# Kernel tuning notes

Hardware: AMD Instinct MI355X
Metric: run time of the kernel (lower is better)

## Reference

```python
import jax, jax.numpy as jnp
import numpy as np

RHO = 1.0
EPSILON = 0.1
N_ITERS = 5
EPS = 1e-08


def setup_inputs() -> dict:
    key = jax.random.key(0)
    k1, k2, k3 = jax.random.split(key, 3)
    B, H, M, N, D = 16, 16, 256, 576, 1024
    # student cross-attention weights: positive, rows roughly sum to 1 (post-softmax in the real model)
    sa = jax.random.uniform(k1, (B, H, M, N), dtype=jnp.float32) + 1e-3
    student_attn = sa / sa.sum(axis=-1, keepdims=True)
    visual_feats = jax.random.normal(k2, (B, N, D), dtype=jnp.float32)
    text_feats = jax.random.normal(k3, (B, M, D), dtype=jnp.float32)
    text_mask = jnp.ones((B, M), dtype=jnp.float32)
    return {"student_attn": student_attn, "visual_feats": visual_feats,
            "text_feats": text_feats, "text_mask": text_mask}


def _l2norm(x):
    return x / jnp.sqrt(jnp.sum(x * x, axis=-1, keepdims=True) + 1e-12)


def _teacher_plan(x, y, y_mask):
    # x: (B,N,D) visual, y: (B,M,D) text, y_mask: (B,M)
    B, N, D = x.shape
    M = y.shape[1]
    x_n = _l2norm(x)
    y_n = _l2norm(y)
    cost = 1.0 - jnp.einsum('bmd,bnd->bmn', y_n, x_n)          # (B,M,N)
    mu = jnp.full((B, N, 1), 1.0 / N, dtype=x.dtype)            # visual marginal (column vec)
    nu = (y_mask / (jnp.sum(y_mask, axis=1, keepdims=True) + EPS))[:, :, None]  # (B,M,1)
    K = jnp.exp(-cost / EPSILON)                                # (B,M,N)
    fi = RHO / (RHO + EPSILON)
    u = jnp.ones((B, M, 1), dtype=x.dtype)
    v = jnp.ones((B, N, 1), dtype=x.dtype)
    for _ in range(N_ITERS):
        Kv = jnp.einsum('bmn,bnk->bmk', K, v)                   # (B,M,1)
        u = (nu / (Kv + EPS)) ** fi
        Ktu = jnp.einsum('bmn,bmk->bnk', K, u)                  # (B,N,1)
        v = (mu / (Ktu + EPS)) ** fi
    P = u * K * jnp.swapaxes(v, 1, 2)                           # (B,M,N)
    return P / (jnp.sum(P, axis=-1, keepdims=True) + EPS)


def reference(student_attn, visual_feats, text_feats, text_mask):
    teacher = jax.lax.stop_gradient(_teacher_plan(visual_feats, text_feats, text_mask))
    teacher = teacher[:, None, :, :]                            # (B,1,M,N)
    loss = -jnp.sum(teacher * jnp.log(student_attn + EPS), axis=-1)  # (B,H,M)
    loss = loss * text_mask[:, None, :]
    return jnp.mean(loss)
```

## Files before the change

kernel.cpp:

```cpp
#include <hip/hip_runtime.h>
#include <math.h>

#define B_ 16
#define H_ 16
#define M_ 256
#define N_ 576
#define D_ 1024

constexpr float EPS_ = 1e-8f;
constexpr float FI_ = 0.90909090909090906f;

__device__ __forceinline__ float wave_reduce(float v) {
#pragma unroll
  for (int o = 32; o > 0; o >>= 1) v += __shfl_down(v, o, 64);
  return v;
}

__global__ __launch_bounds__(256) void rownorm_kernel(const float* __restrict__ x,
                                                      float* __restrict__ inv,
                                                      int rows) {
  int wave = (int)((blockIdx.x * blockDim.x + threadIdx.x) >> 6);
  int lane = threadIdx.x & 63;
  if (wave >= rows) return;
  const float* r = x + (size_t)wave * D_;
  float s = 0.f;
#pragma unroll
  for (int it = 0; it < 4; ++it) {
    float4 v = *(const float4*)&r[it * 256 + lane * 4];
    s += v.x * v.x + v.y * v.y + v.z * v.z + v.w * v.w;
  }
  s = wave_reduce(s);
  if (lane == 0) inv[wave] = rsqrtf(s + 1e-12f);
}

__global__ __launch_bounds__(256) void gemm_k_kernel(const float* __restrict__ vis,
                                                     const float* __restrict__ txt,
                                                     const float* __restrict__ xinv,
                                                     const float* __restrict__ yinv,
                                                     float* __restrict__ Kw) {
  __shared__ float As[16][68];
  __shared__ float Bs[16][68];
  const int b = blockIdx.z;
  const int m0 = blockIdx.y * 64;
  const int n0 = blockIdx.x * 64;
  const float* Y = txt + (size_t)b * M_ * D_;
  const float* X = vis + (size_t)b * N_ * D_;
  const int t = threadIdx.x;
  const int row = t >> 2;
  const int dl = (t & 3) << 2;
  const int tm = (t >> 4) << 2;
  const int tn = (t & 15) << 2;

  float acc[4][4] = {};
  for (int d0 = 0; d0 < D_; d0 += 16) {
    float4 ay = *(const float4*)&Y[(size_t)(m0 + row) * D_ + d0 + dl];
    float4 ax = *(const float4*)&X[(size_t)(n0 + row) * D_ + d0 + dl];
    As[dl + 0][row] = ay.x; As[dl + 1][row] = ay.y;
    As[dl + 2][row] = ay.z; As[dl + 3][row] = ay.w;
    Bs[dl + 0][row] = ax.x; Bs[dl + 1][row] = ax.y;
    Bs[dl + 2][row] = ax.z; Bs[dl + 3][row] = ax.w;
    __syncthreads();
#pragma unroll
    for (int k = 0; k < 16; ++k) {
      float4 a4 = *(const float4*)&As[k][tm];
      float4 b4 = *(const float4*)&Bs[k][tn];
      float a[4] = {a4.x, a4.y, a4.z, a4.w};
      float bb[4] = {b4.x, b4.y, b4.z, b4.w};
#pragma unroll
      for (int i = 0; i < 4; ++i)
#pragma unroll
        for (int j = 0; j < 4; ++j) acc[i][j] += a[i] * bb[j];
    }
    __syncthreads();
  }

  float ym[4], xn[4];
#pragma unroll
  for (int i = 0; i < 4; ++i) {
    ym[i] = yinv[b * M_ + m0 + tm + i];
    xn[i] = xinv[b * N_ + n0 + tn + i];
  }
#pragma unroll
  for (int i = 0; i < 4; ++i) {
    float4 o;
    o.x = expf(10.f * (acc[i][0] * ym[i] * xn[0] - 1.f));
    o.y = expf(10.f * (acc[i][1] * ym[i] * xn[1] - 1.f));
    o.z = expf(10.f * (acc[i][2] * ym[i] * xn[2] - 1.f));
    o.w = expf(10.f * (acc[i][3] * ym[i] * xn[3] - 1.f));
    *(float4*)&Kw[((size_t)b * M_ + m0 + tm + i) * N_ + n0 + tn] = o;
  }
}


__global__ __launch_bounds__(576) void sink_setup(const float* __restrict__ mask,
                                                  float* __restrict__ nu,
                                                  float* __restrict__ v) {
  __shared__ float sh_red[9];
  const int b = blockIdx.x;
  const int t = threadIdx.x;
  float mval = (t < M_) ? mask[b * M_ + t] : 0.f;
  float w = wave_reduce(mval);
  if ((t & 63) == 0) sh_red[t >> 6] = w;
  __syncthreads();
  float summ = 0.f;
#pragma unroll
  for (int i = 0; i < 9; ++i) summ += sh_red[i];
  if (t < M_) nu[b * M_ + t] = mval / (summ + EPS_);
  v[b * N_ + t] = 1.f;
}

__global__ __launch_bounds__(256) void sink_u(const float* __restrict__ Kw,
                                              const float* __restrict__ v,
                                              const float* __restrict__ nu,
                                              float* __restrict__ u) {
  const int b = blockIdx.y;
  const int row = blockIdx.x * 4 + (threadIdx.x >> 6);
  const int lane = threadIdx.x & 63;
  const float* rowp = Kw + ((size_t)b * M_ + row) * N_;
  const float* vb = v + b * N_;
  float s = 0.f;
#pragma unroll
  for (int k = 0; k < 9; ++k) s += rowp[lane + 64 * k] * vb[lane + 64 * k];
  s = wave_reduce(s);
  if (lane == 0) {
    int idx = b * M_ + row;
    u[idx] = powf(nu[idx] / (s + EPS_), FI_);
  }
}

__global__ __launch_bounds__(256) void sink_v(const float* __restrict__ Kw,
                                              const float* __restrict__ u,
                                              float* __restrict__ v) {
  __shared__ float part[4][64];
  const int b = blockIdx.y;
  const int n0 = blockIdx.x * 64;
  const int col = n0 + (threadIdx.x & 63);
  const int g = threadIdx.x >> 6;
  const float* Kb = Kw + (size_t)b * M_ * N_;
  const float* ub = u + b * M_;
  float s = 0.f;
#pragma unroll 8
  for (int m = g * 64; m < (g + 1) * 64; ++m) s += Kb[(size_t)m * N_ + col] * ub[m];
  part[g][threadIdx.x & 63] = s;
  __syncthreads();
  if (threadIdx.x < 64) {
    float tot = part[0][threadIdx.x] + part[1][threadIdx.x] +
                part[2][threadIdx.x] + part[3][threadIdx.x];
    v[b * N_ + n0 + threadIdx.x] = powf((1.f / (float)N_) / (tot + EPS_), FI_);
  }
}

__global__ __launch_bounds__(256) void sink_scale(const float* __restrict__ Kw,
                                                  const float* __restrict__ v,
                                                  const float* __restrict__ u,
                                                  const float* __restrict__ mask,
                                                  float* __restrict__ scale) {
  const int b = blockIdx.y;
  const int row = blockIdx.x * 4 + (threadIdx.x >> 6);
  const int lane = threadIdx.x & 63;
  const float* rowp = Kw + ((size_t)b * M_ + row) * N_;
  const float* vb = v + b * N_;
  float s = 0.f;
#pragma unroll
  for (int k = 0; k < 9; ++k) s += rowp[lane + 64 * k] * vb[lane + 64 * k];
  s = wave_reduce(s);
  if (lane == 0) {
    int idx = b * M_ + row;
    float uu = u[idx];
    scale[idx] = mask[idx] * uu / (uu * s + EPS_);
  }
}

__global__ __launch_bounds__(256) void loss_kernel(const float* __restrict__ student,
                                                   const float* __restrict__ Kw,
                                                   const float* __restrict__ v,
                                                   const float* __restrict__ scale,
                                                   float* __restrict__ out) {
  const unsigned TOT = (unsigned)B_ * H_ * M_ * (N_ / 4);
  __shared__ float sh[4];
  float acc = 0.f;
  for (unsigned idx = blockIdx.x * blockDim.x + threadIdx.x; idx < TOT;
       idx += gridDim.x * blockDim.x) {
    unsigned n4 = idx % (N_ / 4);
    unsigned rem = idx / (N_ / 4);
    unsigned m = rem & (M_ - 1);
    rem >>= 8;
    unsigned b = rem >> 4;
    float4 s4 = *(const float4*)&student[(size_t)idx * 4];
    float4 k4 = *(const float4*)&Kw[(size_t)(b * M_ + m) * N_ + n4 * 4];
    float4 v4 = *(const float4*)&v[(size_t)b * N_ + n4 * 4];
    float sc = scale[b * M_ + m];
    float tsum = k4.x * v4.x * __logf(s4.x + EPS_) + k4.y * v4.y * __logf(s4.y + EPS_) +
                 k4.z * v4.z * __logf(s4.z + EPS_) + k4.w * v4.w * __logf(s4.w + EPS_);
    acc -= sc * tsum;
  }
  float w = wave_reduce(acc);
  int lane = threadIdx.x & 63, wv = threadIdx.x >> 6;
  if (lane == 0) sh[wv] = w;
  __syncthreads();
  if (threadIdx.x == 0) {
    float tot = sh[0] + sh[1] + sh[2] + sh[3];
    atomicAdd(out, tot * (1.f / ((float)B_ * H_ * M_)));
  }
}

extern "C" void kernel_launch(void* const* d_in, const int* in_sizes, int n_in,
                              void* d_out, int out_size, void* d_ws, size_t ws_size,
                              hipStream_t stream) {
  const float* student = (const float*)d_in[0];
  const float* vis = (const float*)d_in[1];
  const float* txt = (const float*)d_in[2];
  const float* mask = (const float*)d_in[3];
  float* out = (float*)d_out;

  char* ws = (char*)d_ws;
  const size_t K_BYTES = (size_t)B_ * M_ * N_ * 4;
  float* Kw = (float*)ws;
  char* p = ws + K_BYTES;
  float* xinv = (float*)p; p += B_ * N_ * 4;
  float* yinv = (float*)p; p += B_ * M_ * 4;
  float* vv = (float*)p;   p += B_ * N_ * 4;
  float* scale = (float*)p; p += B_ * M_ * 4;
  float* nu = (float*)p;   p += B_ * M_ * 4;
  float* uu = (float*)p;   p += B_ * M_ * 4;

  hipMemsetAsync(d_out, 0, sizeof(float), stream);
  rownorm_kernel<<<(B_ * N_) / 4, 256, 0, stream>>>(vis, xinv, B_ * N_);
  rownorm_kernel<<<(B_ * M_) / 4, 256, 0, stream>>>(txt, yinv, B_ * M_);
  gemm_k_kernel<<<dim3(N_ / 64, M_ / 64, B_), 256, 0, stream>>>(vis, txt, xinv, yinv, Kw);

  sink_setup<<<B_, N_, 0, stream>>>(mask, nu, vv);
  for (int it = 0; it < 5; ++it) {
    sink_u<<<dim3(M_ / 4, B_), 256, 0, stream>>>(Kw, vv, nu, uu);
    sink_v<<<dim3(N_ / 64, B_), 256, 0, stream>>>(Kw, uu, vv);
  }
  sink_scale<<<dim3(M_ / 4, B_), 256, 0, stream>>>(Kw, vv, uu, mask, scale);

  loss_kernel<<<4096, 256, 0, stream>>>(student, Kw, vv, scale, out);
}
```

Before: 409.3 us.

## Normalize features to bf16 and compute the cosine GEMM with MFMA

The row-norm kernels now normalize each row and write it out in bf16. The fp32 SIMT outer-product GEMM is replaced by a bf16 MFMA 16x16x32 GEMM with 64x64 tiles that reads those pre-normalized inputs. This removes the fp32 FMA compute bottleneck and halves the operand bytes the GEMM reads. In exchange it adds a bf16 write and read of the full feature tensors and loses precision in the cosine similarity, which gets amplified by exp(10*x). The epilogue now writes K with scalar stores instead of float4 stores.

Result: faster. 349.0 us (-14.7%).

```diff
diff --git a/kernel.cpp b/kernel.cpp
--- a/kernel.cpp
+++ b/kernel.cpp
@@ -6,89 +6,113 @@
 #define M_ 256
 #define N_ 576
 #define D_ 1024
+#define BK 64
+#define LDS_STRIDE (BK + 8)
 
 constexpr float EPS_ = 1e-8f;
 constexpr float FI_ = 0.90909090909090906f;
 
+typedef __bf16 bf16x8 __attribute__((ext_vector_type(8)));
+typedef float f32x4 __attribute__((ext_vector_type(4)));
+
 __device__ __forceinline__ float wave_reduce(float v) {
 #pragma unroll
   for (int o = 32; o > 0; o >>= 1) v += __shfl_down(v, o, 64);
   return v;
 }
 
-__global__ __launch_bounds__(256) void rownorm_kernel(const float* __restrict__ x,
-                                                      float* __restrict__ inv,
-                                                      int rows) {
+__device__ __forceinline__ unsigned short f2bf(float f) {
+  union { float f; unsigned u; } a; a.f = f;
+  unsigned r = a.u + 0x7fff + ((a.u >> 16) & 1);
+  return (unsigned short)(r >> 16);
+}
+
+__global__ __launch_bounds__(256) void norm_bf16_kernel(const float* __restrict__ x,
+                                                        unsigned short* __restrict__ out,
+                                                        int rows) {
   int wave = (int)((blockIdx.x * blockDim.x + threadIdx.x) >> 6);
   int lane = threadIdx.x & 63;
   if (wave >= rows) return;
   const float* r = x + (size_t)wave * D_;
+  float4 v[4];
   float s = 0.f;
 #pragma unroll
   for (int it = 0; it < 4; ++it) {
-    float4 v = *(const float4*)&r[it * 256 + lane * 4];
-    s += v.x * v.x + v.y * v.y + v.z * v.z + v.w * v.w;
+    v[it] = *(const float4*)&r[it * 256 + lane * 4];
+    s += v[it].x * v[it].x + v[it].y * v[it].y + v[it].z * v[it].z + v[it].w * v[it].w;
   }
   s = wave_reduce(s);
-  if (lane == 0) inv[wave] = rsqrtf(s + 1e-12f);
-}
-
-__global__ __launch_bounds__(256) void gemm_k_kernel(const float* __restrict__ vis,
-                                                     const float* __restrict__ txt,
-                                                     const float* __restrict__ xinv,
-                                                     const float* __restrict__ yinv,
-                                                     float* __restrict__ Kw) {
-  __shared__ float As[16][68];
-  __shared__ float Bs[16][68];
+  s = __shfl(s, 0, 64);
+  float inv = rsqrtf(s + 1e-12f);
+  unsigned short* o = out + (size_t)wave * D_;
+#pragma unroll
+  for (int it = 0; it < 4; ++it) {
+    ushort4 pk;
+    pk.x = f2bf(v[it].x * inv);
+    pk.y = f2bf(v[it].y * inv);
+    pk.z = f2bf(v[it].z * inv);
+    pk.w = f2bf(v[it].w * inv);
+    *(ushort4*)&o[it * 256 + lane * 4] = pk;
+  }
+}
+
+__global__ __launch_bounds__(256) void gemm_k_mfma(const unsigned short* __restrict__ xb,
+                                                   const unsigned short* __restrict__ yb,
+                                                   float* __restrict__ Kw) {
+  __shared__ unsigned short As[64][LDS_STRIDE];
+  __shared__ unsigned short Bs[64][LDS_STRIDE];
   const int b = blockIdx.z;
   const int m0 = blockIdx.y * 64;
   const int n0 = blockIdx.x * 64;
-  const float* Y = txt + (size_t)b * M_ * D_;
-  const float* X = vis + (size_t)b * N_ * D_;
+  const unsigned short* Y = yb + (size_t)b * M_ * D_;
+  const unsigned short* X = xb + (size_t)b * N_ * D_;
   const int t = threadIdx.x;
-  const int row = t >> 2;
-  const int dl = (t & 3) << 2;
-  const int tm = (t >> 4) << 2;
-  const int tn = (t & 15) << 2;
-
-  float acc[4][4] = {};
-  for (int d0 = 0; d0 < D_; d0 += 16) {
-    float4 ay = *(const float4*)&Y[(size_t)(m0 + row) * D_ + d0 + dl];
-    float4 ax = *(const float4*)&X[(size_t)(n0 + row) * D_ + d0 + dl];
-    As[dl + 0][row] = ay.x; As[dl + 1][row] = ay.y;
-    As[dl + 2][row] = ay.z; As[dl + 3][row] = ay.w;
-    Bs[dl + 0][row] = ax.x; Bs[dl + 1][row] = ax.y;
-    Bs[dl + 2][row] = ax.z; Bs[dl + 3][row] = ax.w;
-    __syncthreads();
-#pragma unroll
-    for (int k = 0; k < 16; ++k) {
-      float4 a4 = *(const float4*)&As[k][tm];
-      float4 b4 = *(const float4*)&Bs[k][tn];
-      float a[4] = {a4.x, a4.y, a4.z, a4.w};
-      float bb[4] = {b4.x, b4.y, b4.z, b4.w};
-#pragma unroll
-      for (int i = 0; i < 4; ++i)
-#pragma unroll
-        for (int j = 0; j < 4; ++j) acc[i][j] += a[i] * bb[j];
+  const int lane = t & 63;
+  const int w = t >> 6;
+  const int wm = (w & 1) * 32;
+  const int wn = (w >> 1) * 32;
+  const int lr = t >> 3;
+  const int lc = (t & 7) * 8;
+  const int fr = lane & 15;
+  const int fk = (lane >> 4) * 8;
+
+  f32x4 acc[2][2] = {};
+  for (int k0 = 0; k0 < D_; k0 += BK) {
+#pragma unroll
+    for (int p = 0; p < 2; ++p) {
+      *(uint4*)&As[lr + 32 * p][lc] = *(const uint4*)&Y[(size_t)(m0 + lr + 32 * p) * D_ + k0 + lc];
+      *(uint4*)&Bs[lr + 32 * p][lc] = *(const uint4*)&X[(size_t)(n0 + lr + 32 * p) * D_ + k0 + lc];
     }
     __syncthreads();
-  }
-
-  float ym[4], xn[4];
-#pragma unroll
-  for (int i = 0; i < 4; ++i) {
-    ym[i] = yinv[b * M_ + m0 + tm + i];
-    xn[i] = xinv[b * N_ + n0 + tn + i];
-  }
-#pragma unroll
-  for (int i = 0; i < 4; ++i) {
-    float4 o;
-    o.x = expf(10.f * (acc[i][0] * ym[i] * xn[0] - 1.f));
-    o.y = expf(10.f * (acc[i][1] * ym[i] * xn[1] - 1.f));
-    o.z = expf(10.f * (acc[i][2] * ym[i] * xn[2] - 1.f));
-    o.w = expf(10.f * (acc[i][3] * ym[i] * xn[3] - 1.f));
-    *(float4*)&Kw[((size_t)b * M_ + m0 + tm + i) * N_ + n0 + tn] = o;
-  }
+#pragma unroll
+    for (int ks = 0; ks < BK; ks += 32) {
+      bf16x8 a[2], bfr[2];
+#pragma unroll
+      for (int i = 0; i < 2; ++i) {
+        a[i] = *(const bf16x8*)&As[wm + i * 16 + fr][ks + fk];
+        bfr[i] = *(const bf16x8*)&Bs[wn + i * 16 + fr][ks + fk];
+      }
+#pragma unroll
+      for (int i = 0; i < 2; ++i)
+#pragma unroll
+        for (int j = 0; j < 2; ++j)
+          acc[i][j] = __builtin_amdgcn_mfma_f32_16x16x32_bf16(a[i], bfr[j], acc[i][j], 0, 0, 0);
+    }
+    __syncthreads();
+  }
+
+  const int cm = (lane >> 4) * 4;
+  const int cn = lane & 15;
+#pragma unroll
+  for (int i = 0; i < 2; ++i)
+#pragma unroll
+    for (int j = 0; j < 2; ++j)
+#pragma unroll
+      for (int rg = 0; rg < 4; ++rg) {
+        int m = m0 + wm + i * 16 + cm + rg;
+        int n = n0 + wn + j * 16 + cn;
+        Kw[((size_t)b * M_ + m) * N_ + n] = expf(10.f * (acc[i][j][rg] - 1.f));
+      }
 }
 
 
@@ -217,17 +241,17 @@
   const size_t K_BYTES = (size_t)B_ * M_ * N_ * 4;
   float* Kw = (float*)ws;
   char* p = ws + K_BYTES;
-  float* xinv = (float*)p; p += B_ * N_ * 4;
-  float* yinv = (float*)p; p += B_ * M_ * 4;
-  float* vv = (float*)p;   p += B_ * N_ * 4;
+  unsigned short* xb = (unsigned short*)p; p += (size_t)B_ * N_ * D_ * 2;
+  unsigned short* ybf = (unsigned short*)p; p += (size_t)B_ * M_ * D_ * 2;
+  float* vv = (float*)p;    p += B_ * N_ * 4;
   float* scale = (float*)p; p += B_ * M_ * 4;
-  float* nu = (float*)p;   p += B_ * M_ * 4;
-  float* uu = (float*)p;   p += B_ * M_ * 4;
+  float* nu = (float*)p;    p += B_ * M_ * 4;
+  float* uu = (float*)p;    p += B_ * M_ * 4;
 
   hipMemsetAsync(d_out, 0, sizeof(float), stream);
-  rownorm_kernel<<<(B_ * N_) / 4, 256, 0, stream>>>(vis, xinv, B_ * N_);
-  rownorm_kernel<<<(B_ * M_) / 4, 256, 0, stream>>>(txt, yinv, B_ * M_);
-  gemm_k_kernel<<<dim3(N_ / 64, M_ / 64, B_), 256, 0, stream>>>(vis, txt, xinv, yinv, Kw);
+  norm_bf16_kernel<<<(B_ * N_) / 4, 256, 0, stream>>>(vis, xb, B_ * N_);
+  norm_bf16_kernel<<<(B_ * M_) / 4, 256, 0, stream>>>(txt, ybf, B_ * M_);
+  gemm_k_mfma<<<dim3(N_ / 64, M_ / 64, B_), 256, 0, stream>>>(xb, ybf, Kw);
 
   sink_setup<<<B_, N_, 0, stream>>>(mask, nu, vv);
   for (int it = 0; it < 5; ++it) {
```
